# Optimization experiments

Hardware: AMD Instinct MI355X
Metric: run time of the kernel (lower is better)

The kernel has to match this reference:

```python
import jax, jax.numpy as jnp
import numpy as np

SEQ, B, E, HID = 512, 32, 256, 256
H2 = 2 * HID              # BiLSTM output / DAG-LSTM hidden size
R, NE, NS, SW = 128, 64, 64, 8
N = NE + NS               # total node slots (entities + relation nodes)
VOCAB, NEL = 50000, 128
CLAMP_C, CLAMP_H = 100.0, 100.0


def _uni(k, shape, fan_in):
    b = 1.0 / np.sqrt(fan_in)
    return jax.random.uniform(k, shape, jnp.float32, -b, b)


def setup_inputs() -> dict:
    key = jax.random.key(0)
    ks = jax.random.split(key, 24)
    inp = {}
    inp["tokens"] = jax.random.randint(ks[0], (SEQ, B), 0, VOCAB)
    inp["entity_spans"] = jax.random.randint(ks[1], (NE, SW), 0, SEQ)
    inp["element_names"] = jax.random.randint(ks[2], (NS, B), 0, NEL)
    inp["H"] = jnp.zeros((N, B, H2), jnp.float32)
    inp["A"] = jnp.zeros((1,), jnp.int32)  # unused by forward (as in original)
    inp["T"] = jnp.broadcast_to(jnp.arange(NS, dtype=jnp.int32)[:, None] + NE, (NS, B))
    inp["S"] = jax.random.randint(ks[3], (NS, B, 2), 0, NE + 32)
    inp["entity_spans_size"] = jnp.full((B,), NE, jnp.int32)
    # learned parameters
    inp["word_emb"] = jax.random.normal(ks[4], (VOCAB, E), jnp.float32)
    inp["elem_emb"] = jax.random.normal(ks[5], (NEL, R), jnp.float32)
    inp["attn_w"] = _uni(ks[6], (1, H2), H2)
    inp["attn_b"] = _uni(ks[7], (1,), H2)
    inp["Wih_f"] = _uni(ks[8], (4 * HID, E), E)
    inp["Whh_f"] = _uni(ks[9], (4 * HID, HID), HID)
    inp["bl_f"] = _uni(ks[10], (4 * HID,), HID)
    inp["Wih_b"] = _uni(ks[11], (4 * HID, E), E)
    inp["Whh_b"] = _uni(ks[12], (4 * HID, HID), HID)
    inp["bl_b"] = _uni(ks[13], (4 * HID,), HID)
    inp["W_ioc"] = _uni(ks[14], (3 * H2, R), R + 2 * H2)
    inp["U_ioc"] = _uni(ks[15], (3 * H2, 2 * H2), R + 2 * H2)
    inp["b_ioc"] = _uni(ks[16], (3 * H2,), R + 2 * H2)
    inp["Wf"] = _uni(ks[17], (H2, R), R + H2)
    inp["Uf"] = _uni(ks[18], (H2, H2), R + H2)
    inp["bf"] = _uni(ks[19], (H2,), R + H2)
    inp["W1"] = _uni(ks[20], (2 * H2, H2), H2)
    inp["b1"] = _uni(ks[21], (2 * H2,), H2)
    inp["W2"] = _uni(ks[22], (2, 2 * H2), 2 * H2)
    inp["b2"] = _uni(ks[23], (2,), 2 * H2)
    return inp


def _lstm_dir(x, Wih, Whh, b, reverse):
    # x: [seq, batch, E]; torch gate order i, f, g, o
    h0 = jnp.zeros((x.shape[1], Whh.shape[1]), x.dtype)

    def step(carry, xt):
        h, c = carry
        g = xt @ Wih.T + h @ Whh.T + b
        i, f, gg, o = jnp.split(g, 4, axis=-1)
        c = jax.nn.sigmoid(f) * c + jax.nn.sigmoid(i) * jnp.tanh(gg)
        h = jax.nn.sigmoid(o) * jnp.tanh(c)
        return (h, c), h

    xs = x[::-1] if reverse else x
    _, hs = jax.lax.scan(step, (h0, h0), xs)
    return hs[::-1] if reverse else hs


def _forward(tokens, entity_spans, element_names, H, T, S, entity_spans_size,
             word_emb, elem_emb, attn_w, attn_b,
             Wih_f, Whh_f, bl_f, Wih_b, Whh_b, bl_b,
             W_ioc, U_ioc, b_ioc, Wf, Uf, bf, W1, b1, W2, b2):
    emb = word_emb[tokens]                                  # [SEQ,B,E]
    fwd = _lstm_dir(emb, Wih_f, Whh_f, bl_f, False)
    bwd = _lstm_dir(emb, Wih_b, Whh_b, bl_b, True)
    blstm = jnp.concatenate([fwd, bwd], axis=-1)            # [SEQ,B,H2]

    # attention pooling over entity spans; original multiplies the softmax
    # weights (which sum to 1) against blstm_out[i], so h_entity = wsum * blstm[i]
    attn = blstm @ attn_w[0] + attn_b[0]                    # [SEQ,B]
    scores = attn[entity_spans]                             # [NE,SW,B]
    wsum = jax.nn.softmax(scores, axis=1).sum(axis=1)       # [NE,B] (== 1 up to fp)
    ne = entity_spans.shape[0]
    H = H.at[:ne].set(wsum[..., None] * blstm[:ne])

    rej = jnp.array([0.999, 0.001], jnp.float32)
    acc0 = jnp.array([0.001, 0.999], jnp.float32)
    n_nodes = H.shape[0]

    def cell(hv, c, e):
        # DAG-LSTM cell: hv [2,H2] input hiddens, c [H2] shared cell state, e [R]
        ioc = e @ W_ioc.T + hv.reshape(-1) @ U_ioc.T + b_ioc
        i, o, ch = jnp.split(ioc, 3)
        f = jax.nn.sigmoid(e @ Wf.T + hv @ Uf.T + bf)       # [2,H2] per-input forget
        c_new = jnp.clip(jnp.sum(f * c[None, :], axis=0)
                         + jax.nn.sigmoid(i) * jnp.tanh(ch), -CLAMP_C, CLAMP_C)
        h = jnp.clip(jax.nn.sigmoid(o) * jnp.tanh(c_new), -CLAMP_H, CLAMP_H)
        return h, c_new

    P0 = jnp.concatenate([jnp.tile(acc0, (ne, 1)),
                          jnp.zeros((n_nodes - ne, 2), jnp.float32)], axis=0)

    def batch_body(c, xs):
        Hb, Sb, Tb, Eb, ent_sz = xs

        def step(carry, inp):
            Hb, Pb, c = carry
            args, tgt, el = inp
            valid = (tgt >= ent_sz) & (el > -1)
            cond = jnp.all(Pb[args, 1] > 0.5) & valid
            h_out, c_new = cell(Hb[args], c, elem_emb[el])
            logits = W2 @ (W1 @ h_out + b1) + b2
            pred = jnp.where(cond, jax.nn.softmax(logits), rej)
            Hb = Hb.at[tgt].set(jnp.where(cond, h_out, Hb[tgt]))
            c = jnp.where(cond, c_new, c)
            Pb = Pb.at[tgt].set(jnp.where(valid, pred, Pb[tgt]))
            return (Hb, Pb, c), None

        (Hb, Pb, c), _ = jax.lax.scan(step, (Hb, P0, c), (Sb, Tb, Eb))
        return c, Pb

    # cell state c rolls sequentially across batches, matching the torch loop order
    xs = (jnp.swapaxes(H, 0, 1), jnp.swapaxes(S, 0, 1), T.T,
          element_names.T, entity_spans_size)
    _, P = jax.lax.scan(batch_body, jnp.zeros((H.shape[-1],), jnp.float32), xs)
    return P.reshape(-1, 2)


def reference(tokens, entity_spans, element_names, H, A, T, S, entity_spans_size,
              word_emb, elem_emb, attn_w, attn_b,
              Wih_f, Whh_f, bl_f, Wih_b, Whh_b, bl_b,
              W_ioc, U_ioc, b_ioc, Wf, Uf, bf, W1, b1, W2, b2):
    return _forward(tokens, entity_spans, element_names, H, T, S, entity_spans_size,
                    word_emb, elem_emb, attn_w, attn_b,
                    Wih_f, Whh_f, bl_f, Wih_b, Whh_b, bl_b,
                    W_ioc, U_ioc, b_ioc, Wf, Uf, bf, W1, b1, W2, b2)
```

## Files before the change

kernel.cpp:

```cpp
#include <hip/hip_runtime.h>
#include <stdint.h>

#define SEQB 512
#define BATCH 32
#define EDIM 256
#define HIDN 256
#define HH2 512
#define RDIM 128
#define NEnt 64
#define NSt 64
#define NNODE 128
#define NHELP 112
#define HPG 14
#define NROWS 3584
#define TERMEVT 0xFFFFFFFFu
#define SCOPE_AGENT __HIP_MEMORY_SCOPE_AGENT

static __device__ __forceinline__ float sigm(float x) { return 1.0f / (1.0f + __expf(-x)); }
static __device__ __forceinline__ float tanh_f(float x) { return 1.0f - 2.0f / (__expf(2.0f * x) + 1.0f); }

static __device__ __forceinline__ void barrier_lds() {
  asm volatile("s_waitcnt lgkmcnt(0)" ::: "memory");
  __builtin_amdgcn_sched_barrier(0);
  __builtin_amdgcn_s_barrier();
}

template<int GATHER, int BIASFIRST>
__global__ __launch_bounds__(256) void gemm_tn(
    const float* __restrict__ A, const int* __restrict__ gidx, const float* __restrict__ gtab,
    const float* __restrict__ B0, const float* __restrict__ B1, int nsplitB,
    const float* __restrict__ bias0, const float* __restrict__ bias1, int nsplitBias,
    float* __restrict__ C, int M, int N, int K)
{
  __shared__ float As[16][132];
  __shared__ float Bs[16][132];
  const int tid = threadIdx.x;
  const int m0 = blockIdx.y * 128, n0 = blockIdx.x * 128;

  const int lrow = tid >> 1;
  const int lk   = (tid & 1) * 8;
  const float* arow;
  if (GATHER) arow = gtab + (size_t)gidx[m0 + lrow] * K + lk;
  else        arow = A + (size_t)(m0 + lrow) * K + lk;
  const int bn = n0 + lrow;
  const float* brow = ((bn < nsplitB) ? (B0 + (size_t)bn * K)
                                      : (B1 + (size_t)(bn - nsplitB) * K)) + lk;

  const int tx = tid & 15, ty = tid >> 4;

  float bb[2][4];
#pragma unroll
  for (int in = 0; in < 2; ++in)
#pragma unroll
    for (int j = 0; j < 4; ++j) bb[in][j] = 0.f;
  if (bias0) {
#pragma unroll
    for (int in = 0; in < 2; ++in)
#pragma unroll
      for (int j = 0; j < 4; ++j) {
        int n = n0 + in * 64 + tx * 4 + j;
        bb[in][j] = (n < nsplitBias) ? bias0[n] : bias1[n - nsplitBias];
      }
  }

  float acc[2][2][4][4];
#pragma unroll
  for (int im = 0; im < 2; ++im)
#pragma unroll
    for (int in = 0; in < 2; ++in)
#pragma unroll
      for (int i = 0; i < 4; ++i)
#pragma unroll
        for (int j = 0; j < 4; ++j)
          acc[im][in][i][j] = BIASFIRST ? bb[in][j] : 0.f;

  float4 pa0 = *(const float4*)(arow);
  float4 pa1 = *(const float4*)(arow + 4);
  float4 pb0 = *(const float4*)(brow);
  float4 pb1 = *(const float4*)(brow + 4);

  int k0 = 0;
  while (true) {
    __syncthreads();
    As[lk + 0][lrow] = pa0.x; As[lk + 1][lrow] = pa0.y;
    As[lk + 2][lrow] = pa0.z; As[lk + 3][lrow] = pa0.w;
    As[lk + 4][lrow] = pa1.x; As[lk + 5][lrow] = pa1.y;
    As[lk + 6][lrow] = pa1.z; As[lk + 7][lrow] = pa1.w;
    Bs[lk + 0][lrow] = pb0.x; Bs[lk + 1][lrow] = pb0.y;
    Bs[lk + 2][lrow] = pb0.z; Bs[lk + 3][lrow] = pb0.w;
    Bs[lk + 4][lrow] = pb1.x; Bs[lk + 5][lrow] = pb1.y;
    Bs[lk + 6][lrow] = pb1.z; Bs[lk + 7][lrow] = pb1.w;
    __syncthreads();

    k0 += 16;
    const bool more = (k0 < K);
    if (more) {
      pa0 = *(const float4*)(arow + k0);
      pa1 = *(const float4*)(arow + k0 + 4);
      pb0 = *(const float4*)(brow + k0);
      pb1 = *(const float4*)(brow + k0 + 4);
    }

#pragma unroll
    for (int k = 0; k < 16; ++k) {
      const float4 av0 = *(const float4*)&As[k][ty * 4];
      const float4 av1 = *(const float4*)&As[k][64 + ty * 4];
      const float4 bv0 = *(const float4*)&Bs[k][tx * 4];
      const float4 bv1 = *(const float4*)&Bs[k][64 + tx * 4];
      const float am[2][4] = {{av0.x, av0.y, av0.z, av0.w},
                              {av1.x, av1.y, av1.z, av1.w}};
      const float bw[2][4] = {{bv0.x, bv0.y, bv0.z, bv0.w},
                              {bv1.x, bv1.y, bv1.z, bv1.w}};
#pragma unroll
      for (int im = 0; im < 2; ++im)
#pragma unroll
        for (int in = 0; in < 2; ++in)
#pragma unroll
          for (int i = 0; i < 4; ++i)
#pragma unroll
            for (int j = 0; j < 4; ++j)
              acc[im][in][i][j] += am[im][i] * bw[in][j];
    }
    if (!more) break;
  }

#pragma unroll
  for (int im = 0; im < 2; ++im)
#pragma unroll
    for (int i = 0; i < 4; ++i) {
      const int m = m0 + im * 64 + ty * 4 + i;
#pragma unroll
      for (int in = 0; in < 2; ++in) {
        float4 o;
        o.x = acc[im][in][i][0] + (BIASFIRST ? 0.f : bb[in][0]);
        o.y = acc[im][in][i][1] + (BIASFIRST ? 0.f : bb[in][1]);
        o.z = acc[im][in][i][2] + (BIASFIRST ? 0.f : bb[in][2]);
        o.w = acc[im][in][i][3] + (BIASFIRST ? 0.f : bb[in][3]);
        *(float4*)&C[(size_t)m * N + n0 + in * 64 + tx * 4] = o;
      }
    }
}

__global__ __launch_bounds__(256, 1) void lstm_esplit(
    const float* __restrict__ Xg,
    const float* __restrict__ Whh_f, const float* __restrict__ Whh_b,
    unsigned long long* __restrict__ hxbuf,
    float* __restrict__ blstm)
{
  const int tid = threadIdx.x;
  const int pid = blockIdx.x;
  const int q = pid >> 6, chain = pid & 63;
  const int d = chain >> 5, b = chain & 31;
  const int j = tid & 63;
  const int g = tid >> 6;
  const int elem = q * 64 + j;
  const int grow = g * 256 + elem;

  const float* W = (d ? Whh_b : Whh_f) + (size_t)grow * 256;
  float4 w4[64];
#pragma unroll
  for (int i = 0; i < 64; ++i) w4[i] = *(const float4*)(W + 4 * i);

  __shared__ float h_lds[HIDN];
  __shared__ float gsL[256];
  float creg = 0.f;
  h_lds[tid] = 0.f;
  __syncthreads();

  const float4* h4 = (const float4*)h_lds;
  const int pe = (tid < q * 64) ? tid : (tid + 64);
  const size_t xgoff = (size_t)d * 1024 + grow;

  for (int it = 0; it < SEQB; ++it) {
    const int t = d ? (SEQB - 1 - it) : it;
    const size_t m = (size_t)t * BATCH + b;
    const float xv = Xg[m * 2048 + xgoff];

    if (tid < 192) {
      const unsigned long long* src =
          &hxbuf[((size_t)(it & 1) * 64 + chain) * 256 + pe];
      unsigned long long qv;
      do { qv = __hip_atomic_load(src, __ATOMIC_RELAXED, SCOPE_AGENT); }
      while ((unsigned)(qv >> 32) != (unsigned)it);
      h_lds[pe] = __uint_as_float((unsigned)qv);
    }
    barrier_lds();

    float a0 = 0.f, a1 = 0.f, a2 = 0.f, a3 = 0.f;
#pragma unroll
    for (int i = 0; i < 64; ++i) {
      const float4 hv = h4[i];
      const float4 wv = w4[i];
      a0 += wv.x * hv.x; a1 += wv.y * hv.y; a2 += wv.z * hv.z; a3 += wv.w * hv.w;
    }
    gsL[tid] = (a0 + a1) + (a2 + a3) + xv;
    barrier_lds();

    if (tid < 64) {
      const float gi = gsL[tid], gf = gsL[64 + tid];
      const float gg = gsL[128 + tid], go = gsL[192 + tid];
      creg = sigm(gf) * creg + sigm(gi) * tanh_f(gg);
      const float hn = sigm(go) * tanh_f(creg);
      h_lds[elem] = hn;
      const unsigned long long pk =
          ((unsigned long long)(unsigned)(it + 1) << 32) |
          (unsigned long long)__float_as_uint(hn);
      __hip_atomic_store(&hxbuf[((size_t)((it + 1) & 1) * 64 + chain) * 256 + elem], pk,
                         __ATOMIC_RELAXED, SCOPE_AGENT);
      blstm[m * HH2 + (size_t)d * HIDN + elem] = hn;
    }
    barrier_lds();
  }
}

__global__ __launch_bounds__(256) void attn_k(const float* __restrict__ blstm,
                                              const float* __restrict__ attn_w,
                                              const float* __restrict__ attn_b,
                                              float* __restrict__ attnv)
{
  const int tid = threadIdx.x;
  const int p = blockIdx.x * 4 + (tid >> 6);
  const int lane = tid & 63;
  const size_t base = (size_t)p * HH2 + lane * 8;
  float4 v0 = *(const float4*)&blstm[base];
  float4 v1 = *(const float4*)&blstm[base + 4];
  float4 w0 = *(const float4*)&attn_w[lane * 8];
  float4 w1 = *(const float4*)&attn_w[lane * 8 + 4];
  float acc = v0.x * w0.x + v0.y * w0.y + v0.z * w0.z + v0.w * w0.w
            + v1.x * w1.x + v1.y * w1.y + v1.z * w1.z + v1.w * w1.w;
#pragma unroll
  for (int off = 32; off > 0; off >>= 1) acc += __shfl_down(acc, off);
  if (lane == 0) attnv[p] = acc + attn_b[0];
}

__global__ __launch_bounds__(64) void entity_prep(const int* __restrict__ spans,
                                                  const float* __restrict__ attnv,
                                                  const float* __restrict__ blstm,
                                                  float* __restrict__ Hent,
                                                  float* __restrict__ P_out)
{
  const int nb = blockIdx.x;
  const int n = nb >> 5, b = nb & 31;
  const int tid = threadIdx.x;
  __shared__ float sc[8];
  if (tid < 8) sc[tid] = attnv[spans[n * 8 + tid] * BATCH + b];
  __syncthreads();
  float mx = sc[0];
#pragma unroll
  for (int w = 1; w < 8; ++w) mx = fmaxf(mx, sc[w]);
  float ex[8]; float ssum = 0.f;
#pragma unroll
  for (int w = 0; w < 8; ++w) { ex[w] = __expf(sc[w] - mx); ssum += ex[w]; }
  float wsum = 0.f;
#pragma unroll
  for (int w = 0; w < 8; ++w) wsum += ex[w] / ssum;
  const size_t base = ((size_t)n * BATCH + b) * HH2;
#pragma unroll
  for (int q = 0; q < 2; ++q) {
    int j = q * 256 + tid * 4;
    float4 v = *(const float4*)&blstm[base + j];
    v.x *= wsum; v.y *= wsum; v.z *= wsum; v.w *= wsum;
    *(float4*)&Hent[base + j] = v;
  }
  if (tid == 0) {
    P_out[((size_t)b * NNODE + n) * 2 + 0] = 0.001f;
    P_out[((size_t)b * NNODE + n) * 2 + 1] = 0.999f;
  }
}

__global__ void pack_ucat(const float* __restrict__ U_ioc, const float* __restrict__ Uf,
                          float* __restrict__ Ucat)
{
  int j = blockIdx.x, tid = threadIdx.x;
  for (int k = tid; k < 512; k += 128) {
    float v;
    if (j < 1536)      v = U_ioc[(size_t)j * 1024 + k];
    else if (j < 3072) v = U_ioc[(size_t)(j - 1536) * 1024 + 512 + k];
    else               v = Uf[(size_t)(j - 3072) * 512 + k];
    Ucat[(size_t)j * 512 + k] = v;
  }
}

__global__ __launch_bounds__(256) void mprep(const float* __restrict__ W1,
                                             const float* __restrict__ b1,
                                             const float* __restrict__ W2,
                                             const float* __restrict__ b2,
                                             float* __restrict__ Mmat,
                                             float* __restrict__ mbv)
{
  const int tid = threadIdx.x;
  for (int j = tid; j < 512; j += 256) {
    float a0 = 0.f, a1 = 0.f;
    for (int m = 0; m < 1024; ++m) {
      float w = W1[(size_t)m * 512 + j];
      a0 += W2[m] * w;
      a1 += W2[1024 + m] * w;
    }
    Mmat[j] = a0; Mmat[512 + j] = a1;
  }
  if (tid < 2) {
    float a = b2[tid];
    for (int m = 0; m < 1024; ++m) a += W2[tid * 1024 + m] * b1[m];
    mbv[tid] = a;
  }
}

__global__ __launch_bounds__(512) void dag_seq(
    const int* __restrict__ S, const int* __restrict__ T, const int* __restrict__ EN,
    const int* __restrict__ entsz,
    const float* __restrict__ WE,
    const float* __restrict__ Mmat, const float* __restrict__ mbv,
    float* __restrict__ Tall, float* __restrict__ hbuf,
    uint32_t* head, uint32_t* slotbase, uint32_t* arrive,
    const float* __restrict__ Ucat, float* __restrict__ P_out)
{
  const int tid = threadIdx.x;
  __shared__ int   SL[NSt * BATCH * 2];
  __shared__ int   TLt[NSt * BATCH];
  __shared__ int   ELt[NSt * BATCH];
  __shared__ int   eszL[BATCH];
  __shared__ float MmatL[1024];
  __shared__ float mbvL[2];
  __shared__ float pstL[NNODE];
  __shared__ int   evtofL[NSt];
  __shared__ int   confL[NSt];
  __shared__ float red0[8], red1[8], bcast[2];
  __shared__ uint32_t sslot;

  if (blockIdx.x < NHELP) {
    const int w = blockIdx.x;
    const int row = w * 32 + (tid >> 4);
    const int ks = (tid & 15) * 32;
    float wreg[32];
#pragma unroll
    for (int i = 0; i < 8; ++i) {
      float4 v = *(const float4*)&Ucat[(size_t)row * 512 + ks + i * 4];
      wreg[i * 4 + 0] = v.x; wreg[i * 4 + 1] = v.y; wreg[i * 4 + 2] = v.z; wreg[i * 4 + 3] = v.w;
    }
    uint32_t done = 0;
    const int g = w & 7;
    while (true) {
      if (tid == 0) {
        while (__hip_atomic_load(head, __ATOMIC_RELAXED, SCOPE_AGENT) <= done) {
          __builtin_amdgcn_s_sleep(4);
        }
        __builtin_amdgcn_fence(__ATOMIC_ACQUIRE, "agent");
        sslot = slotbase[done];
      }
      __syncthreads();
      const uint32_t slot = sslot;
      if (slot == TERMEVT) break;
      const float* hv = hbuf + (size_t)done * HH2 + ks;
      float acc = 0.f;
#pragma unroll
      for (int i = 0; i < 8; ++i) {
        float4 v = *(const float4*)&hv[i * 4];
        acc += wreg[i * 4 + 0] * v.x + wreg[i * 4 + 1] * v.y
             + wreg[i * 4 + 2] * v.z + wreg[i * 4 + 3] * v.w;
      }
      acc += __shfl_down(acc, 8);
      acc += __shfl_down(acc, 4);
      acc += __shfl_down(acc, 2);
      acc += __shfl_down(acc, 1);
      if ((tid & 15) == 0) {
        __hip_atomic_store(&Tall[(size_t)slot + row], acc, __ATOMIC_RELAXED, SCOPE_AGENT);
      }
      __syncthreads();
      if (tid == 0) {
        __hip_atomic_fetch_add(&arrive[done * 8 + g], 1u, __ATOMIC_RELEASE, SCOPE_AGENT);
      }
      ++done;
    }
    return;
  }

  for (int i = tid; i < NSt * BATCH * 2; i += 512) SL[i] = S[i];
  for (int i = tid; i < NSt * BATCH; i += 512) { TLt[i] = T[i]; ELt[i] = EN[i]; }
  for (int i = tid; i < 1024; i += 512) MmatL[i] = Mmat[i];
  if (tid < BATCH) eszL[tid] = entsz[tid];
  if (tid < 2) mbvL[tid] = mbv[tid];
  __syncthreads();

  float c = 0.f;
  uint32_t e = 0;
  for (int b = 0; b < BATCH; ++b) {
    const int esz = eszL[b];
    for (int j = tid; j < NNODE; j += 512) pstL[j] = (j < NEnt) ? 0.999f : 0.f;
    if (tid < NSt) confL[tid] = 0;
    __syncthreads();

    bool  pfok = false;
    float pt0 = 0.f, pt1 = 0.f, pt2 = 0.f, pt3 = 0.f, pt4 = 0.f, pt5 = 0.f, pt6 = 0.f, pt7 = 0.f;
    float pw0 = 0.f, pw1 = 0.f, pw2 = 0.f, pwf = 0.f;

#define PFETCH(sn)                                                              \
    do {                                                                        \
      pfok = false;                                                             \
      if ((sn) < NSt) {                                                         \
        const int sbn_ = (sn) * BATCH + b;                                      \
        const int na0_ = SL[2 * sbn_], na1_ = SL[2 * sbn_ + 1];                 \
        const int nel_ = ELt[sbn_];                                             \
        if (nel_ >= 0) {                                                        \
          const float* nwe_ = WE + (size_t)nel_ * 2048;                         \
          pw0 = nwe_[tid]; pw1 = nwe_[512 + tid]; pw2 = nwe_[1024 + tid];       \
          pwf = nwe_[1536 + tid];                                               \
        }                                                                       \
        const bool ok0_ = (na0_ < NEnt) || (confL[na0_ - NEnt] != 0);           \
        const bool ok1_ = (na1_ < NEnt) || (confL[na1_ - NEnt] != 0);           \
        if (ok0_ && ok1_) {                                                     \
          const size_t ns0_ = ((size_t)na0_ * BATCH + b) * NROWS;               \
          const size_t ns1_ = ((size_t)na1_ * BATCH + b) * NROWS;               \
          pt0 = Tall[ns0_ + tid];               pt1 = Tall[ns1_ + 1536 + tid];  \
          pt2 = Tall[ns0_ + 512 + tid];         pt3 = Tall[ns1_ + 2048 + tid];  \
          pt4 = Tall[ns0_ + 1024 + tid];        pt5 = Tall[ns1_ + 2560 + tid];  \
          pt6 = Tall[ns0_ + 3072 + tid];        pt7 = Tall[ns1_ + 3072 + tid];  \
          pfok = true;                                                          \
        }                                                                       \
      }                                                                         \
    } while (0)

    PFETCH(0);

    for (int s = 0; s < NSt; ++s) {
      const int sb = s * BATCH + b;
      const int a0 = SL[2 * sb], a1 = SL[2 * sb + 1];
      const int tgt = TLt[sb], el = ELt[sb];
      const bool valid = (tgt >= esz) && (el > -1);
      const float pa0 = pstL[a0], pa1 = pstL[a1];
      const bool cond = valid && (pa0 > 0.5f) && (pa1 > 0.5f);
      if (cond) {
        if (!pfok) {
          const int r0 = (a0 >= NEnt) ? (a0 - NEnt) : -1;
          const int r1 = (a1 >= NEnt) ? (a1 - NEnt) : -1;
          if (tid < 8 && r0 >= 0 && !confL[r0]) {
            const uint32_t ev = (uint32_t)evtofL[r0];
            while (__hip_atomic_load(&arrive[ev * 8 + tid], __ATOMIC_RELAXED, SCOPE_AGENT)
                   < (uint32_t)HPG) { __builtin_amdgcn_s_sleep(1); }
          }
          if (tid >= 8 && tid < 16 && r1 >= 0 && !confL[r1]) {
            const uint32_t ev = (uint32_t)evtofL[r1];
            while (__hip_atomic_load(&arrive[ev * 8 + (tid - 8)], __ATOMIC_RELAXED, SCOPE_AGENT)
                   < (uint32_t)HPG) { __builtin_amdgcn_s_sleep(1); }
          }
          __syncthreads();
          if (tid == 0) {
            __builtin_amdgcn_fence(__ATOMIC_ACQUIRE, "agent");
            if (r0 >= 0) confL[r0] = 1;
            if (r1 >= 0) confL[r1] = 1;
          }
          __syncthreads();
          const size_t s0 = ((size_t)a0 * BATCH + b) * NROWS;
          const size_t s1 = ((size_t)a1 * BATCH + b) * NROWS;
          pt0 = Tall[s0 + tid];        pt1 = Tall[s1 + 1536 + tid];
          pt2 = Tall[s0 + 512 + tid];  pt3 = Tall[s1 + 2048 + tid];
          pt4 = Tall[s0 + 1024 + tid]; pt5 = Tall[s1 + 2560 + tid];
          pt6 = Tall[s0 + 3072 + tid]; pt7 = Tall[s1 + 3072 + tid];
        }
        const float ii = pw0 + pt0 + pt1;
        const float oo = pw1 + pt2 + pt3;
        const float ch = pw2 + pt4 + pt5;
        const float f0 = sigm(pwf + pt6);
        const float f1 = sigm(pwf + pt7);
        PFETCH(s + 1);
        float cn = (f0 + f1) * c + sigm(ii) * tanh_f(ch);
        cn = fminf(fmaxf(cn, -100.f), 100.f);
        float hh = sigm(oo) * tanh_f(cn);
        hh = fminf(fmaxf(hh, -100.f), 100.f);
        float l0 = MmatL[tid] * hh, l1 = MmatL[512 + tid] * hh;
#pragma unroll
        for (int off = 32; off > 0; off >>= 1) {
          l0 += __shfl_down(l0, off);
          l1 += __shfl_down(l1, off);
        }
        if ((tid & 63) == 0) { red0[tid >> 6] = l0; red1[tid >> 6] = l1; }
        barrier_lds();
        if (tid == 0) {
          float L0 = mbvL[0], L1 = mbvL[1];
#pragma unroll
          for (int wv = 0; wv < 8; ++wv) { L0 += red0[wv]; L1 += red1[wv]; }
          float mx = fmaxf(L0, L1);
          float e0 = __expf(L0 - mx), e1 = __expf(L1 - mx);
          float inv = 1.f / (e0 + e1);
          const float o0 = e0 * inv, o1 = e1 * inv;
          bcast[0] = o0; bcast[1] = o1;
          pstL[tgt] = o1;
          P_out[((size_t)b * NNODE + tgt) * 2 + 0] = o0;
          P_out[((size_t)b * NNODE + tgt) * 2 + 1] = o1;
        }
        barrier_lds();
        c = cn;
        const bool pub = (bcast[1] > 0.5f) && (tgt < NEnt + 32);
        if (pub) {
          __hip_atomic_store(&hbuf[(size_t)e * HH2 + tid], hh, __ATOMIC_RELAXED, SCOPE_AGENT);
          __syncthreads();
          if (tid == 0) {
            evtofL[tgt - NEnt] = (int)e;
            __hip_atomic_store(&slotbase[e], (uint32_t)(((uint32_t)tgt * BATCH + (uint32_t)b) * NROWS),
                               __ATOMIC_RELAXED, SCOPE_AGENT);
            __hip_atomic_store(head, e + 1u, __ATOMIC_RELEASE, SCOPE_AGENT);
          }
          ++e;
          barrier_lds();
        }
      } else {
        PFETCH(s + 1);
        if (tid == 0) {
          const float o0 = valid ? 0.999f : ((tgt < NEnt) ? 0.001f : 0.f);
          const float o1 = valid ? 0.001f : ((tgt < NEnt) ? 0.999f : 0.f);
          if (valid || tgt >= NEnt) {
            P_out[((size_t)b * NNODE + tgt) * 2 + 0] = o0;
            P_out[((size_t)b * NNODE + tgt) * 2 + 1] = o1;
          }
          if (valid) pstL[tgt] = o1;
        }
        barrier_lds();
      }
    }
#undef PFETCH
  }
  if (tid == 0) {
    __hip_atomic_store(&slotbase[e], TERMEVT, __ATOMIC_RELAXED, SCOPE_AGENT);
    __hip_atomic_store(head, e + 1u, __ATOMIC_RELEASE, SCOPE_AGENT);
  }
}

extern "C" void kernel_launch(void* const* d_in, const int* in_sizes, int n_in,
                              void* d_out, int out_size, void* d_ws, size_t ws_size,
                              hipStream_t stream)
{
  const int* tokens = (const int*)d_in[0];
  const int* spans  = (const int*)d_in[1];
  const int* enames = (const int*)d_in[2];
  const int* T      = (const int*)d_in[5];
  const int* S      = (const int*)d_in[6];
  const int* entsz  = (const int*)d_in[7];
  const float* word_emb = (const float*)d_in[8];
  const float* elem_emb = (const float*)d_in[9];
  const float* attn_w = (const float*)d_in[10];
  const float* attn_b = (const float*)d_in[11];
  const float* Wih_f = (const float*)d_in[12];
  const float* Whh_f = (const float*)d_in[13];
  const float* bl_f  = (const float*)d_in[14];
  const float* Wih_b = (const float*)d_in[15];
  const float* Whh_b = (const float*)d_in[16];
  const float* bl_b  = (const float*)d_in[17];
  const float* W_ioc = (const float*)d_in[18];
  const float* U_ioc = (const float*)d_in[19];
  const float* b_ioc = (const float*)d_in[20];
  const float* Wf    = (const float*)d_in[21];
  const float* Uf    = (const float*)d_in[22];
  const float* bf    = (const float*)d_in[23];
  const float* W1    = (const float*)d_in[24];
  const float* b1    = (const float*)d_in[25];
  const float* W2    = (const float*)d_in[26];
  const float* b2    = (const float*)d_in[27];
  float* P_out = (float*)d_out;

  char* ws = (char*)d_ws;
  uint32_t* head     = (uint32_t*)ws;
  uint32_t* slotbase = (uint32_t*)(ws + 8192);
  uint32_t* arrive   = (uint32_t*)(ws + 16384);
  float* fws = (float*)(ws + 65536);
  size_t off = 0;
  float* Xg    = fws + off; off += (size_t)16384 * 2048;
  float* blstm = fws + off; off += (size_t)SEQB * BATCH * HH2;
  float* attnv = fws + off; off += (size_t)SEQB * BATCH;
  float* Hent  = fws + off; off += (size_t)2048 * 512;
  float* Tall  = fws + off; off += (size_t)96 * BATCH * NROWS;
  unsigned long long* hxbuf = (unsigned long long*)(fws + off);
  off += (size_t)2 * 64 * 256 * 2;
  float* Ucat  = fws + off; off += (size_t)NROWS * 512;
  float* WE    = fws + off; off += (size_t)128 * 2048;
  float* Mmat  = fws + off; off += 1024;
  float* mbv   = fws + off; off += 16;
  float* hbuf  = fws + off; off += (size_t)1024 * 512;
  const size_t needed = 65536 + off * sizeof(float);
  if (ws_size < needed) return;

  hipMemsetAsync(d_ws, 0, 65536, stream);
  hipMemsetAsync(hxbuf, 0, (size_t)2 * 64 * 256 * 8, stream);

  gemm_tn<1, 0><<<dim3(2048 / 128, 16384 / 128), 256, 0, stream>>>(
      nullptr, tokens, word_emb, Wih_f, Wih_b, 1024, bl_f, bl_b, 1024,
      Xg, 16384, 2048, 256);

  lstm_esplit<<<256, 256, 0, stream>>>(Xg, Whh_f, Whh_b, hxbuf, blstm);

  attn_k<<<4096, 256, 0, stream>>>(blstm, attn_w, attn_b, attnv);
  entity_prep<<<2048, 64, 0, stream>>>(spans, attnv, blstm, Hent, P_out);

  pack_ucat<<<NROWS, 128, 0, stream>>>(U_ioc, Uf, Ucat);
  gemm_tn<0, 1><<<dim3(2048 / 128, 1), 256, 0, stream>>>(
      elem_emb, nullptr, nullptr, W_ioc, Wf, 1536, b_ioc, bf, 1536,
      WE, 128, 2048, 128);
  mprep<<<1, 256, 0, stream>>>(W1, b1, W2, b2, Mmat, mbv);
  gemm_tn<0, 0><<<dim3(NROWS / 128, 2048 / 128), 256, 0, stream>>>(
      Hent, nullptr, nullptr, Ucat, nullptr, 0x40000000, nullptr, nullptr, 0,
      Tall, 2048, NROWS, 512);

  dag_seq<<<NHELP + 1, 512, 0, stream>>>(S, T, enames, entsz, WE, Mmat, mbv,
                                         Tall, hbuf, head, slotbase, arrive, Ucat, P_out);
}
```

Baseline: 5.489 ms.

## Remove per-step barriers in DAG-LSTM scan via double-buffered reductions and redundant softmax

Double-buffers the cross-wave reduction scratch so every thread computes the 2-way softmax itself. This drops the broadcast barrier after the softmax and the barrier in the rejected-step branch, with each wave writing its own pstL entry. It also marks as confirmed every relation node whose publish event is no later than one already waited on, so later steps skip redundant spin-waits on the helper blocks. A barrier is added at the start of each batch so resets stay safe. Correctness now rests on subtler LDS ordering, since several waves write the same pstL entry and other threads read it without a barrier.

```diff
diff --git a/kernel.cpp b/kernel.cpp
--- a/kernel.cpp
+++ b/kernel.cpp
@@ -324,7 +324,7 @@
   __shared__ float pstL[NNODE];
   __shared__ int   evtofL[NSt];
   __shared__ int   confL[NSt];
-  __shared__ float red0[8], red1[8], bcast[2];
+  __shared__ float red0[2][8], red1[2][8];
   __shared__ uint32_t sslot;
 
   if (blockIdx.x < NHELP) {
@@ -384,10 +384,12 @@
   float c = 0.f;
   uint32_t e = 0;
   for (int b = 0; b < BATCH; ++b) {
+    barrier_lds();
     const int esz = eszL[b];
     for (int j = tid; j < NNODE; j += 512) pstL[j] = (j < NEnt) ? 0.999f : 0.f;
-    if (tid < NSt) confL[tid] = 0;
+    if (tid < NSt) { confL[tid] = 0; evtofL[tid] = -1; }
     __syncthreads();
+    int fp = 0;
 
     bool  pfok = false;
     float pt0 = 0.f, pt1 = 0.f, pt2 = 0.f, pt3 = 0.f, pt4 = 0.f, pt5 = 0.f, pt6 = 0.f, pt7 = 0.f;
@@ -445,8 +447,15 @@
           __syncthreads();
           if (tid == 0) {
             __builtin_amdgcn_fence(__ATOMIC_ACQUIRE, "agent");
-            if (r0 >= 0) confL[r0] = 1;
-            if (r1 >= 0) confL[r1] = 1;
+            int evm = -1;
+            if (r0 >= 0) { confL[r0] = 1; if (evtofL[r0] > evm) evm = evtofL[r0]; }
+            if (r1 >= 0) { confL[r1] = 1; if (evtofL[r1] > evm) evm = evtofL[r1]; }
+            if (evm >= 0) {
+              for (int r = 0; r < 32; ++r) {
+                const int ev_ = evtofL[r];
+                if (ev_ >= 0 && ev_ <= evm) confL[r] = 1;
+              }
+            }
           }
           __syncthreads();
           const size_t s0 = ((size_t)a0 * BATCH + b) * NROWS;
@@ -472,24 +481,23 @@
           l0 += __shfl_down(l0, off);
           l1 += __shfl_down(l1, off);
         }
-        if ((tid & 63) == 0) { red0[tid >> 6] = l0; red1[tid >> 6] = l1; }
+        if ((tid & 63) == 0) { red0[fp][tid >> 6] = l0; red1[fp][tid >> 6] = l1; }
         barrier_lds();
+        float L0 = mbvL[0], L1 = mbvL[1];
+#pragma unroll
+        for (int wv = 0; wv < 8; ++wv) { L0 += red0[fp][wv]; L1 += red1[fp][wv]; }
+        const float mx = fmaxf(L0, L1);
+        const float e0 = __expf(L0 - mx), e1 = __expf(L1 - mx);
+        const float inv = 1.f / (e0 + e1);
+        const float o0 = e0 * inv, o1 = e1 * inv;
+        if ((tid & 63) == 0) pstL[tgt] = o1;
         if (tid == 0) {
-          float L0 = mbvL[0], L1 = mbvL[1];
-#pragma unroll
-          for (int wv = 0; wv < 8; ++wv) { L0 += red0[wv]; L1 += red1[wv]; }
-          float mx = fmaxf(L0, L1);
-          float e0 = __expf(L0 - mx), e1 = __expf(L1 - mx);
-          float inv = 1.f / (e0 + e1);
-          const float o0 = e0 * inv, o1 = e1 * inv;
-          bcast[0] = o0; bcast[1] = o1;
-          pstL[tgt] = o1;
           P_out[((size_t)b * NNODE + tgt) * 2 + 0] = o0;
           P_out[((size_t)b * NNODE + tgt) * 2 + 1] = o1;
         }
-        barrier_lds();
+        fp ^= 1;
         c = cn;
-        const bool pub = (bcast[1] > 0.5f) && (tgt < NEnt + 32);
+        const bool pub = (o1 > 0.5f) && (tgt < NEnt + 32);
         if (pub) {
           __hip_atomic_store(&hbuf[(size_t)e * HH2 + tid], hh, __ATOMIC_RELAXED, SCOPE_AGENT);
           __syncthreads();
@@ -504,16 +512,13 @@
         }
       } else {
         PFETCH(s + 1);
-        if (tid == 0) {
+        if (tid == 0 && (valid || tgt >= NEnt)) {
           const float o0 = valid ? 0.999f : ((tgt < NEnt) ? 0.001f : 0.f);
           const float o1 = valid ? 0.001f : ((tgt < NEnt) ? 0.999f : 0.f);
-          if (valid || tgt >= NEnt) {
-            P_out[((size_t)b * NNODE + tgt) * 2 + 0] = o0;
-            P_out[((size_t)b * NNODE + tgt) * 2 + 1] = o1;
-          }
-          if (valid) pstL[tgt] = o1;
+          P_out[((size_t)b * NNODE + tgt) * 2 + 0] = o0;
+          P_out[((size_t)b * NNODE + tgt) * 2 + 1] = o1;
         }
-        barrier_lds();
+        if (valid && (tid & 63) == 0) pstL[tgt] = 0.001f;
       }
     }
 #undef PFETCH
```

New measurement: 5.462 ms. About the same (-0.5%).
